# Performance work log

Measured on AMD Instinct MI355X. Metric: run time of the kernel, lower is better.

Reference implementation:

```python
import jax, jax.numpy as jnp
import numpy as np

H = 512

def setup_inputs() -> dict:
    key = jax.random.key(0)
    k1, k2, k3, k4 = jax.random.split(key, 4)
    B, S_dec, S_enc = 8, 2048, 2048
    encoder_output = jax.random.normal(k1, (B, S_enc, H), dtype=jnp.float32)
    decoder_output = jax.random.normal(k2, (B, S_dec, H), dtype=jnp.float32)
    # nn.Bilinear(H, H, 1): weight [1, H, H], bias [1]; init U(-1/sqrt(H), 1/sqrt(H))
    bound = 1.0 / np.sqrt(H)
    W = jax.random.uniform(k3, (1, H, H), dtype=jnp.float32, minval=-bound, maxval=bound)
    b = jax.random.uniform(k4, (1,), dtype=jnp.float32, minval=-bound, maxval=bound)
    return {"encoder_output": encoder_output, "decoder_output": decoder_output, "W": W, "b": b}

def reference(encoder_output, decoder_output, W, b):
    # Original: scores[b,d,e] = Bilinear(enc[b,e], dec[b,d]) = enc[b,e] @ W[0] @ dec[b,d] + bias
    # Computed as two GEMMs instead of expanding to [B, S_dec, S_enc, H].
    encW = jnp.einsum('beh,hg->beg', encoder_output, W[0])   # [B, S_enc, H]
    scores = jnp.einsum('beg,bdg->bde', encW, decoder_output) + b[0]  # [B, S_dec, S_enc]
    return scores
```

## Files before the change

### kernel.cpp

```cpp
#include <hip/hip_runtime.h>

typedef __attribute__((ext_vector_type(8))) short short8;
typedef __attribute__((ext_vector_type(4))) float f32x4;
typedef __attribute__((ext_vector_type(8))) unsigned short ushort8;

__device__ __forceinline__ unsigned short f2bf(float x) {
  union { float f; unsigned u; } v; v.f = x;
  unsigned r = v.u + 0x7fffu + ((v.u >> 16) & 1u);
  return (unsigned short)(r >> 16);
}

__global__ __launch_bounds__(256) void wt_kernel(
    const float* __restrict__ W, unsigned short* __restrict__ Wt) {
  __shared__ float s[64][65];
  int g0 = blockIdx.x * 64, h0 = blockIdx.y * 64;
  int tx = threadIdx.x & 63, ty = threadIdx.x >> 6;
#pragma unroll
  for (int rr = 0; rr < 16; ++rr) {
    int h = ty * 16 + rr;
    s[h][tx] = W[(long)(h0 + h) * 512 + g0 + tx];
  }
  __syncthreads();
#pragma unroll
  for (int rr = 0; rr < 16; ++rr) {
    int g = ty * 16 + rr;
    Wt[(long)(g0 + g) * 512 + h0 + tx] = f2bf(s[tx][g]);
  }
}

__global__ __launch_bounds__(256) void gemm1_plus_cvtdec(
    const float* __restrict__ enc, const unsigned short* __restrict__ Wt,
    unsigned short* __restrict__ encW,
    const float* __restrict__ dec, unsigned short* __restrict__ dec_bf) {
  if (blockIdx.x >= 512) {
    int i = (blockIdx.x - 512) * 256 + threadIdx.x;
    const float4* p = (const float4*)(dec + (long)i * 8);
    float4 a = p[0], b = p[1];
    ushort8 o;
    o[0] = f2bf(a.x); o[1] = f2bf(a.y); o[2] = f2bf(a.z); o[3] = f2bf(a.w);
    o[4] = f2bf(b.x); o[5] = f2bf(b.y); o[6] = f2bf(b.z); o[7] = f2bf(b.w);
    *(ushort8*)(dec_bf + (long)i * 8) = o;
    return;
  }

  constexpr int K = 512, N = 512, BK = 32;
  __shared__ __align__(16) short As[128 * BK];
  __shared__ __align__(16) short Bs[128 * BK];

  const int g = blockIdx.x;
  const int work = (g & 7) * 64 + (g >> 3);
  const int bxm = work >> 2, byn = work & 3;

  const int tid = threadIdx.x;
  const int wave = tid >> 6, lane = tid & 63;
  const int wm = wave >> 1, wn = wave & 1;
  const int r = lane & 15, q = lane >> 4;

  const float* Ab = enc + (long)bxm * 128 * K;
  const unsigned short* Bb = Wt + (long)byn * 128 * K;

  const int srow = tid >> 1, shalf = tid & 1;
  const float* arow = Ab + (long)srow * K + shalf * 16;

  f32x4 acc[4][4] = {};
  float4 av[4];
#pragma unroll
  for (int j = 0; j < 4; ++j) av[j] = ((const float4*)arow)[j];

  for (int kt = 0; kt < K; kt += BK) {
    ushort8 o0, o1;
    o0[0] = f2bf(av[0].x); o0[1] = f2bf(av[0].y); o0[2] = f2bf(av[0].z); o0[3] = f2bf(av[0].w);
    o0[4] = f2bf(av[1].x); o0[5] = f2bf(av[1].y); o0[6] = f2bf(av[1].z); o0[7] = f2bf(av[1].w);
    o1[0] = f2bf(av[2].x); o1[1] = f2bf(av[2].y); o1[2] = f2bf(av[2].z); o1[3] = f2bf(av[2].w);
    o1[4] = f2bf(av[3].x); o1[5] = f2bf(av[3].y); o1[6] = f2bf(av[3].z); o1[7] = f2bf(av[3].w);
    *(ushort8*)&As[srow * BK + shalf * 16 + 0] = o0;
    *(ushort8*)&As[srow * BK + shalf * 16 + 8] = o1;

#pragma unroll
    for (int j = 0; j < 2; ++j) {
      int c = (j * 4 + wave) * 64 + lane;
      int row = c >> 2;
      int coff = (c & 3) * 8;
      __builtin_amdgcn_global_load_lds(
          (const __attribute__((address_space(1))) void*)(Bb + (long)row * K + kt + coff),
          (__attribute__((address_space(3))) void*)(Bs + (j * 4 + wave) * 512),
          16, 0, 0);
    }
    __syncthreads();

    short8 af[4], bfr[4];
#pragma unroll
    for (int m = 0; m < 4; ++m)
      af[m] = *(const short8*)&As[(wm * 64 + m * 16 + r) * BK + q * 8];
#pragma unroll
    for (int n = 0; n < 4; ++n)
      bfr[n] = *(const short8*)&Bs[(wn * 64 + n * 16 + r) * BK + q * 8];

    if (kt + BK < K) {
      const float* ap = arow + kt + BK;
#pragma unroll
      for (int j = 0; j < 4; ++j) av[j] = ((const float4*)ap)[j];
    }

#pragma unroll
    for (int m = 0; m < 4; ++m)
#pragma unroll
      for (int n = 0; n < 4; ++n)
        acc[m][n] = __builtin_amdgcn_mfma_f32_16x16x32_bf16(af[m], bfr[n], acc[m][n], 0, 0, 0);
    __syncthreads();
  }

  const long rowbase = (long)bxm * 128 + wm * 64;
  const long colbase = (long)byn * 128 + wn * 64;
#pragma unroll
  for (int m = 0; m < 4; ++m)
#pragma unroll
    for (int n = 0; n < 4; ++n)
#pragma unroll
      for (int j = 0; j < 4; ++j) {
        long row = rowbase + m * 16 + q * 4 + j;
        long col = colbase + n * 16 + r;
        encW[row * (long)N + col] = f2bf(acc[m][n][j]);
      }
}


#define VMCNT(n) asm volatile("s_waitcnt vmcnt(" #n ")" ::: "memory")

#define STAGE(GP, LBASE, tt, kkv)                                             \
  do {                                                                        \
    _Pragma("unroll") for (int j_ = 0; j_ < 2; ++j_) {                        \
      int c_ = w * 2 + j_;                                                    \
      __builtin_amdgcn_global_load_lds(                                       \
          (const __attribute__((address_space(1))) void*)(                    \
              (GP) + ((long)(c_ * 16 + srow)) * 512 + (tt) * 64 + (kkv) * 32 + scol), \
          (__attribute__((address_space(3))) void*)((LBASE) + (c_ << 10)),    \
          16, 0, 0);                                                          \
    }                                                                         \
  } while (0)

#define PHASE(Ac, Bc, kkv, mb, LOADB, STAGE_STMT, ENDWAIT_STMT)               \
  do {                                                                        \
    if (LOADB) {                                                              \
      _Pragma("unroll") for (int n_ = 0; n_ < 4; ++n_)                        \
        bf[kkv][n_] = *(const short8*)((Bc) + (kkv) * 16384 +                 \
                                       ((wn * 4 + n_) << 10) + lconst);       \
    }                                                                         \
    _Pragma("unroll") for (int i_ = 0; i_ < 4; ++i_)                          \
      af[i_] = *(const short8*)((Ac) + (kkv) * 16384 +                        \
                                ((wm * 8 + (mb) + i_) << 10) + lconst);       \
    STAGE_STMT;                                                               \
    __builtin_amdgcn_s_barrier();                                             \
    asm volatile("s_waitcnt lgkmcnt(0)" ::: "memory");                        \
    __builtin_amdgcn_sched_barrier(0);                                        \
    __builtin_amdgcn_s_setprio(1);                                            \
    _Pragma("unroll") for (int i_ = 0; i_ < 4; ++i_)                          \
      _Pragma("unroll") for (int n_ = 0; n_ < 4; ++n_)                        \
        acc[(mb) + i_][n_] = __builtin_amdgcn_mfma_f32_16x16x32_bf16(         \
            af[i_], bf[kkv][n_], acc[(mb) + i_][n_], 0, 0, 0);                \
    __builtin_amdgcn_s_setprio(0);                                            \
    ENDWAIT_STMT;                                                             \
    __builtin_amdgcn_s_barrier();                                             \
  } while (0)

__global__ __launch_bounds__(512, 2) void gemm2_8ph(
    const unsigned short* __restrict__ A,
    const unsigned short* __restrict__ Bt,
    float* __restrict__ C, const float* __restrict__ bias) {
  __shared__ __align__(16) char Lds[131072];
#define LDS_A(d) (Lds + (d) * 32768)
#define LDS_B(d) (Lds + 65536 + (d) * 32768)

  int flat = blockIdx.x;
  int sw = (flat & 7) * 64 + (flat >> 3);
  int z = sw >> 6, xy = sw & 63, bx = xy & 7, by = xy >> 3;

  const int tid = threadIdx.x;
  const int w = tid >> 6, lane = tid & 63;
  const int wm = w >> 2, wn = w & 3;
  const int base_r = lane & 15, q = lane >> 4;
  const int lconst = base_r * 64 + ((q * 16) ^ ((base_r & 8) << 2));
  const int srow = lane >> 2;
  const int scol = ((lane & 3) * 8) ^ (((lane >> 5) & 1) << 4);

  const unsigned short* Ab = A + ((long)z * 2048 + bx * 256) * 512;
  const unsigned short* Bb = Bt + ((long)z * 2048 + by * 256) * 512;

  f32x4 acc[8][4] = {};
  short8 af[4];
  short8 bf[2][4];

  STAGE(Ab, LDS_A(0), 0, 0);
  STAGE(Bb, LDS_B(0), 0, 0);
  STAGE(Ab, LDS_A(0) + 16384, 0, 1);
  STAGE(Bb, LDS_B(0) + 16384, 0, 1);
  VMCNT(4);
  __builtin_amdgcn_s_barrier();

  for (int t = 0; t < 7; ++t) {
    const char* Ac = LDS_A(t & 1);
    const char* Bc = LDS_B(t & 1);
    char* An = LDS_A((t + 1) & 1);
    char* Bn = LDS_B((t + 1) & 1);
    PHASE(Ac, Bc, 0, 0, true,  STAGE(Ab, An, t + 1, 0),         (void)0);
    PHASE(Ac, Bc, 0, 4, false, STAGE(Bb, Bn, t + 1, 0),         VMCNT(4));
    PHASE(Ac, Bc, 1, 0, true,  STAGE(Ab, An + 16384, t + 1, 1), (void)0);
    PHASE(Ac, Bc, 1, 4, false, STAGE(Bb, Bn + 16384, t + 1, 1), VMCNT(4));
  }
  {
    const char* Ac = LDS_A(1);
    const char* Bc = LDS_B(1);
    PHASE(Ac, Bc, 0, 0, true,  (void)0, (void)0);
    PHASE(Ac, Bc, 0, 4, false, (void)0, VMCNT(0));
    PHASE(Ac, Bc, 1, 0, true,  (void)0, (void)0);
    PHASE(Ac, Bc, 1, 4, false, (void)0, (void)0);
  }

  const float bv = bias[0];
  float* Cb = C + ((long)z * 2048 + bx * 256 + wm * 128) * 2048 + by * 256 + wn * 64;
#pragma unroll
  for (int m = 0; m < 8; ++m)
#pragma unroll
    for (int n = 0; n < 4; ++n)
#pragma unroll
      for (int j = 0; j < 4; ++j)
        Cb[(long)(m * 16 + q * 4 + j) * 2048 + n * 16 + base_r] = acc[m][n][j] + bv;
#undef LDS_A
#undef LDS_B
}

extern "C" void kernel_launch(void* const* d_in, const int* in_sizes, int n_in,
                              void* d_out, int out_size, void* d_ws, size_t ws_size,
                              hipStream_t stream) {
  const float* enc  = (const float*)d_in[0];
  const float* dec  = (const float*)d_in[1];
  const float* W    = (const float*)d_in[2];
  const float* bias = (const float*)d_in[3];
  float* out = (float*)d_out;

  constexpr int Bn = 8, S = 2048, H = 512;
  constexpr long NE = (long)Bn * S * H;

  unsigned short* dec_bf = (unsigned short*)d_ws;
  unsigned short* Wt     = dec_bf + NE;
  unsigned short* encW   = Wt + (long)H * H;

  wt_kernel<<<dim3(8, 8), 256, 0, stream>>>(W, Wt);

  gemm1_plus_cvtdec<<<dim3(512 + 4096, 1, 1), 256, 0, stream>>>(
      enc, Wt, encW, dec, dec_bf);

  gemm2_8ph<<<dim3(512, 1, 1), 512, 0, stream>>>(dec_bf, encW, out, bias);
}
```

Baseline: 83.47 us.

## Restructure GEMM2 pipeline into quadrant-based 8-phase schedule with half-tile staging

Reorganizes the second GEMM's main loop so each wave computes 4x2 quadrants of its output using both k-slices per phase. Global-to-LDS staging is split by row-halves, so the next tile's halves can be issued while the current quadrants compute. The block-index swizzle changes to interleave batches across consecutive blocks, and the occupancy hint of 2 blocks per CU is dropped. This is meant to improve overlap of loads with MFMA and raise reuse of register fragments, at the cost of more complex barrier and wait ordering.

```diff
diff --git a/kernel.cpp b/kernel.cpp
--- a/kernel.cpp
+++ b/kernel.cpp
@@ -124,56 +124,64 @@
       }
 }
 
-
 #define VMCNT(n) asm volatile("s_waitcnt vmcnt(" #n ")" ::: "memory")
-
-#define STAGE(GP, LBASE, tt, kkv)                                             \
+#define LGKM0  asm volatile("s_waitcnt lgkmcnt(0)" ::: "memory")
+#define BAR __builtin_amdgcn_s_barrier()
+
+#define LA(p, h) (Lds + (p) * 32768 + (h) * 16384)
+#define LB(p, h) (Lds + 65536 + (p) * 32768 + (h) * 16384)
+
+#define STGH(GP, LBASE, T, H)                                                 \
   do {                                                                        \
     _Pragma("unroll") for (int j_ = 0; j_ < 2; ++j_) {                        \
       int c_ = w * 2 + j_;                                                    \
       __builtin_amdgcn_global_load_lds(                                       \
           (const __attribute__((address_space(1))) void*)(                    \
-              (GP) + ((long)(c_ * 16 + srow)) * 512 + (tt) * 64 + (kkv) * 32 + scol), \
+              (GP) + ((long)((H) * 128 + (c_ >> 1) * 16 + srow)) * 512 +      \
+              (T) * 64 + (c_ & 1) * 32 + scol),                               \
           (__attribute__((address_space(3))) void*)((LBASE) + (c_ << 10)),    \
           16, 0, 0);                                                          \
     }                                                                         \
   } while (0)
 
-#define PHASE(Ac, Bc, kkv, mb, LOADB, STAGE_STMT, ENDWAIT_STMT)               \
+#define LOADAF(p, mh)                                                         \
+  _Pragma("unroll") for (int mi_ = 0; mi_ < 4; ++mi_)                         \
+    _Pragma("unroll") for (int ks_ = 0; ks_ < 2; ++ks_)                       \
+      af[mi_][ks_] = *(const short8*)(LA(p, wm) +                             \
+          ((((mh) * 4 + mi_) * 2 + ks_) << 10) + lconst)
+
+#define LOADBF(p, nh)                                                         \
+  _Pragma("unroll") for (int n_ = 0; n_ < 2; ++n_)                            \
+    _Pragma("unroll") for (int ks_ = 0; ks_ < 2; ++ks_)                       \
+      bf[nh][n_][ks_] = *(const short8*)(LB(p, wn >> 1) +                     \
+          ((((wn & 1) * 4 + (nh) * 2 + n_) * 2 + ks_) << 10) + lconst)
+
+#define QMFMA(mh, nh)                                                         \
   do {                                                                        \
-    if (LOADB) {                                                              \
-      _Pragma("unroll") for (int n_ = 0; n_ < 4; ++n_)                        \
-        bf[kkv][n_] = *(const short8*)((Bc) + (kkv) * 16384 +                 \
-                                       ((wn * 4 + n_) << 10) + lconst);       \
-    }                                                                         \
-    _Pragma("unroll") for (int i_ = 0; i_ < 4; ++i_)                          \
-      af[i_] = *(const short8*)((Ac) + (kkv) * 16384 +                        \
-                                ((wm * 8 + (mb) + i_) << 10) + lconst);       \
-    STAGE_STMT;                                                               \
-    __builtin_amdgcn_s_barrier();                                             \
-    asm volatile("s_waitcnt lgkmcnt(0)" ::: "memory");                        \
+    BAR;                                                                      \
+    LGKM0;                                                                    \
     __builtin_amdgcn_sched_barrier(0);                                        \
     __builtin_amdgcn_s_setprio(1);                                            \
-    _Pragma("unroll") for (int i_ = 0; i_ < 4; ++i_)                          \
-      _Pragma("unroll") for (int n_ = 0; n_ < 4; ++n_)                        \
-        acc[(mb) + i_][n_] = __builtin_amdgcn_mfma_f32_16x16x32_bf16(         \
-            af[i_], bf[kkv][n_], acc[(mb) + i_][n_], 0, 0, 0);                \
+    _Pragma("unroll") for (int mi_ = 0; mi_ < 4; ++mi_)                       \
+      _Pragma("unroll") for (int n_ = 0; n_ < 2; ++n_)                        \
+        _Pragma("unroll") for (int ks_ = 0; ks_ < 2; ++ks_)                   \
+          acc[(mh) * 4 + mi_][(nh) * 2 + n_] =                                \
+              __builtin_amdgcn_mfma_f32_16x16x32_bf16(                        \
+                  af[mi_][ks_], bf[nh][n_][ks_],                              \
+                  acc[(mh) * 4 + mi_][(nh) * 2 + n_], 0, 0, 0);               \
     __builtin_amdgcn_s_setprio(0);                                            \
-    ENDWAIT_STMT;                                                             \
-    __builtin_amdgcn_s_barrier();                                             \
   } while (0)
 
-__global__ __launch_bounds__(512, 2) void gemm2_8ph(
+__global__ __launch_bounds__(512) void gemm2_8ph2(
     const unsigned short* __restrict__ A,
     const unsigned short* __restrict__ Bt,
     float* __restrict__ C, const float* __restrict__ bias) {
   __shared__ __align__(16) char Lds[131072];
-#define LDS_A(d) (Lds + (d) * 32768)
-#define LDS_B(d) (Lds + 65536 + (d) * 32768)
-
-  int flat = blockIdx.x;
-  int sw = (flat & 7) * 64 + (flat >> 3);
-  int z = sw >> 6, xy = sw & 63, bx = xy & 7, by = xy >> 3;
+
+  const int flat = blockIdx.x;
+  const int z = flat & 7;
+  const int work = flat >> 3;
+  const int by = work & 7, bx = work >> 3;
 
   const int tid = threadIdx.x;
   const int w = tid >> 6, lane = tid & 63;
@@ -187,34 +195,55 @@
   const unsigned short* Bb = Bt + ((long)z * 2048 + by * 256) * 512;
 
   f32x4 acc[8][4] = {};
-  short8 af[4];
-  short8 bf[2][4];
-
-  STAGE(Ab, LDS_A(0), 0, 0);
-  STAGE(Bb, LDS_B(0), 0, 0);
-  STAGE(Ab, LDS_A(0) + 16384, 0, 1);
-  STAGE(Bb, LDS_B(0) + 16384, 0, 1);
+  short8 af[4][2];
+  short8 bf[2][2][2];
+
+  STGH(Bb, LB(0, 0), 0, 0);
+  STGH(Bb, LB(0, 1), 0, 1);
+  STGH(Ab, LA(0, 0), 0, 0);
+  STGH(Ab, LA(0, 1), 0, 1);
+  STGH(Bb, LB(1, 0), 1, 0);
+  STGH(Ab, LA(1, 0), 1, 0);
   VMCNT(4);
-  __builtin_amdgcn_s_barrier();
-
-  for (int t = 0; t < 7; ++t) {
-    const char* Ac = LDS_A(t & 1);
-    const char* Bc = LDS_B(t & 1);
-    char* An = LDS_A((t + 1) & 1);
-    char* Bn = LDS_B((t + 1) & 1);
-    PHASE(Ac, Bc, 0, 0, true,  STAGE(Ab, An, t + 1, 0),         (void)0);
-    PHASE(Ac, Bc, 0, 4, false, STAGE(Bb, Bn, t + 1, 0),         VMCNT(4));
-    PHASE(Ac, Bc, 1, 0, true,  STAGE(Ab, An + 16384, t + 1, 1), (void)0);
-    PHASE(Ac, Bc, 1, 4, false, STAGE(Bb, Bn + 16384, t + 1, 1), VMCNT(4));
-  }
-  {
-    const char* Ac = LDS_A(1);
-    const char* Bc = LDS_B(1);
-    PHASE(Ac, Bc, 0, 0, true,  (void)0, (void)0);
-    PHASE(Ac, Bc, 0, 4, false, (void)0, VMCNT(0));
-    PHASE(Ac, Bc, 1, 0, true,  (void)0, (void)0);
-    PHASE(Ac, Bc, 1, 4, false, (void)0, (void)0);
-  }
+  BAR;
+
+  for (int t = 0; t < 3; ++t) {
+    const int T1v = 2 * t + 1, T2v = 2 * t + 2, T3v = 2 * t + 3;
+    LOADAF(0, 0); LOADBF(0, 0);
+    STGH(Ab, LA(1, 1), T1v, 1);
+    QMFMA(0, 0); BAR;
+    LOADBF(0, 1);
+    STGH(Bb, LB(1, 1), T1v, 1);
+    QMFMA(0, 1); BAR;
+    LOADAF(0, 1);
+    STGH(Bb, LB(0, 0), T2v, 0);
+    QMFMA(1, 0); BAR;
+    STGH(Bb, LB(0, 1), T2v, 1);
+    QMFMA(1, 1); VMCNT(4); BAR;
+    LOADAF(1, 0); LOADBF(1, 0);
+    STGH(Ab, LA(0, 0), T2v, 0);
+    QMFMA(0, 0); BAR;
+    LOADBF(1, 1);
+    STGH(Ab, LA(0, 1), T2v, 1);
+    QMFMA(0, 1); BAR;
+    LOADAF(1, 1);
+    STGH(Bb, LB(1, 0), T3v, 0);
+    QMFMA(1, 0); BAR;
+    STGH(Ab, LA(1, 0), T3v, 0);
+    QMFMA(1, 1); VMCNT(4); BAR;
+  }
+  LOADAF(0, 0); LOADBF(0, 0);
+  STGH(Ab, LA(1, 1), 7, 1);
+  QMFMA(0, 0); BAR;
+  LOADBF(0, 1);
+  STGH(Bb, LB(1, 1), 7, 1);
+  QMFMA(0, 1); BAR;
+  LOADAF(0, 1);               QMFMA(1, 0); BAR;
+                              QMFMA(1, 1); VMCNT(0); BAR;
+  LOADAF(1, 0); LOADBF(1, 0); QMFMA(0, 0); BAR;
+  LOADBF(1, 1);               QMFMA(0, 1); BAR;
+  LOADAF(1, 1);               QMFMA(1, 0); BAR;
+                              QMFMA(1, 1);
 
   const float bv = bias[0];
   float* Cb = C + ((long)z * 2048 + bx * 256 + wm * 128) * 2048 + by * 256 + wn * 64;
@@ -225,8 +254,6 @@
 #pragma unroll
       for (int j = 0; j < 4; ++j)
         Cb[(long)(m * 16 + q * 4 + j) * 2048 + n * 16 + base_r] = acc[m][n][j] + bv;
-#undef LDS_A
-#undef LDS_B
 }
 
 extern "C" void kernel_launch(void* const* d_in, const int* in_sizes, int n_in,
@@ -250,5 +277,5 @@
   gemm1_plus_cvtdec<<<dim3(512 + 4096, 1, 1), 256, 0, stream>>>(
       enc, Wt, encW, dec, dec_bf);
 
-  gemm2_8ph<<<dim3(512, 1, 1), 512, 0, stream>>>(dec_bf, encW, out, bias);
-}
+  gemm2_8ph2<<<dim3(512, 1, 1), 512, 0, stream>>>(dec_bf, encW, out, bias);
+}
```

New measurement: 79.57 us (median of 3 runs). 4.7% less time.
